# Optimization experiments

Measured on AMD Instinct MI355X. Metric: run time of the kernel, lower is better.

The kernel has to match this reference:

```python
import jax, jax.numpy as jnp
import numpy as np

K = 7            # kernel_size (odd)
R = K // 2       # neighborhood radius
NH = 16          # num_heads


def _starts(L):
    """NATTEN (dilation=1) window start and rpb start per query index."""
    i = jnp.arange(L)
    win = jnp.clip(i - R, 0, L - K)  # key-window start (window clamped inside image)
    pb = jnp.where(i < R, 2 * R - i, jnp.where(i + R >= L, L - 1 - i, R))
    return win, pb


def setup_inputs() -> dict:
    key = jax.random.key(0)
    ks = jax.random.split(key, 12)
    B, H, W, C = 2, 128, 128, 512
    std = 0.02
    return {
        "q": jax.random.normal(ks[0], (B, H, W, C), jnp.float32),
        "k": jax.random.normal(ks[1], (B, H, W, C), jnp.float32),
        "v": jax.random.normal(ks[2], (B, H, W, C), jnp.float32),
        "wq": jax.random.normal(ks[3], (C, C), jnp.float32) * std,
        "bq": jnp.zeros((C,), jnp.float32),
        "wk": jax.random.normal(ks[4], (C, C), jnp.float32) * std,
        "bk": jnp.zeros((C,), jnp.float32),
        "wv": jax.random.normal(ks[5], (C, C), jnp.float32) * std,
        "bv": jnp.zeros((C,), jnp.float32),
        "rpb": jax.random.normal(ks[6], (NH, 2 * K - 1, 2 * K - 1), jnp.float32) * std,
        "wo": jax.random.normal(ks[7], (C, C), jnp.float32) * std,
        "bo": jnp.zeros((C,), jnp.float32),
    }


def reference(q, k, v, wq, bq, wk, bk, wv, bv, rpb, wo, bo):
    B, H, W, C = q.shape
    hd = C // NH
    scale = hd ** -0.5

    def proj(x, w, b):
        y = x @ w.T + b  # torch nn.Linear
        return y.reshape(B, H, W, NH, hd).transpose(0, 3, 1, 2, 4)  # [B,nh,H,W,hd]

    qh = proj(q, wq, bq) * scale
    kh = proj(k, wk, bk)
    vh = proj(v, wv, bv)

    # H,W (128) >= window_size (7): torch padding branch is dead and omitted.
    sh, ph = _starts(H)
    sw, pw = _starts(W)

    # natten2dqkrpb: per-offset shifted-row/col gathers; never materialize
    # the dense [B,nh,H,W,k*k,hd] unfold.
    logits = []
    for a in range(K):
        kh_a = kh[:, :, sh + a]          # [B,nh,H,W,hd]
        rpb_a = rpb[:, ph + a]           # [nh,H,2K-1]
        for b in range(K):
            k_ab = kh_a[:, :, :, sw + b]             # [B,nh,H,W,hd]
            bias = rpb_a[:, :, pw + b]               # [nh,H,W]
            logits.append(jnp.einsum("bnhwd,bnhwd->bnhw", qh, k_ab) + bias[None])
    attn = jax.nn.softmax(jnp.stack(logits, axis=-1), axis=-1)  # [B,nh,H,W,K*K]

    # natten2dav
    x = jnp.zeros_like(qh)
    for a in range(K):
        vh_a = vh[:, :, sh + a]
        for b in range(K):
            v_ab = vh_a[:, :, :, sw + b]
            x = x + attn[..., a * K + b, None] * v_ab

    x = x.transpose(0, 2, 3, 1, 4).reshape(B, H, W, C)
    return x @ wo.T + bo
```

## Files before the change

kernel.cpp:

```cpp
#include <hip/hip_runtime.h>
#include <hip/hip_bf16.h>

typedef __attribute__((ext_vector_type(8))) _Float16       h8;
typedef __attribute__((ext_vector_type(2))) _Float16       h2;
typedef __attribute__((ext_vector_type(8))) unsigned short u16x8;
typedef __attribute__((ext_vector_type(4))) float          f4;
typedef __attribute__((ext_vector_type(4))) unsigned int   u32x4;
typedef __attribute__((ext_vector_type(2))) unsigned int   u32x2;

__device__ __forceinline__ h2 bch2(unsigned int w) { return __builtin_bit_cast(h2, w); }
__device__ __forceinline__ unsigned int pkrtz(float a, float b) {
    auto r = __builtin_amdgcn_cvt_pkrtz(a, b);
    return __builtin_bit_cast(unsigned int, r);
}
__device__ __forceinline__ void gload_lds16(const void* g, void* l) {
    __builtin_amdgcn_global_load_lds(
        (const __attribute__((address_space(1))) unsigned int*)g,
        (__attribute__((address_space(3))) unsigned int*)l, 16, 0, 0);
}

__global__ __launch_bounds__(256) void cvt_w4(const float* __restrict__ a,
                                              const float* __restrict__ b,
                                              const float* __restrict__ c,
                                              const float* __restrict__ d,
                                              unsigned short* __restrict__ o) {
    const int i   = (blockIdx.x * 256 + threadIdx.x) * 8;
    const int seg = i >> 18;
    const int off = i & 262143;
    const float* s = (seg == 0) ? a : (seg == 1) ? b : (seg == 2) ? c : d;
    f4 x0 = *(const f4*)(s + off);
    f4 x1 = *(const f4*)(s + off + 4);
    u32x4 t;
    t[0] = pkrtz(x0[0], x0[1]);
    t[1] = pkrtz(x0[2], x0[3]);
    t[2] = pkrtz(x1[0], x1[1]);
    t[3] = pkrtz(x1[2], x1[3]);
    *(u32x4*)(o + i) = t;
}

template <bool AF32, bool OF32>
__device__ __forceinline__ void gemm_body(const void* __restrict__ Ap,
                                          const unsigned short* __restrict__ Wb,
                                          const float* __restrict__ bias,
                                          void* __restrict__ Outp,
                                          float scale,
                                          unsigned char* lds) {
    constexpr int KD = 512, BK = 32, NT = KD / BK;
    constexpr int ASZ = AF32 ? 64 * BK * 4 : 64 * BK * 2;
    constexpr int WSZ = 512 * BK * 2;
    constexpr int STRIDE = ASZ + WSZ;

    const int tid  = threadIdx.x;
    const int lane = tid & 63;
    const int w    = tid >> 6;
    const size_t m0 = (size_t)blockIdx.x * 64;

    const float*          Af = (const float*)Ap;
    const unsigned short* Ab = (const unsigned short*)Ap;

    const int fr = lane & 15;
    const int j4 = lane >> 4;

    f4 acc[4][8];
#pragma unroll
    for (int i = 0; i < 4; ++i)
#pragma unroll
        for (int j = 0; j < 8; ++j) acc[i][j] = (f4)(0.0f);

    auto stage = [&](int t, int buf) {
        const int kt = t * BK;
        unsigned char* base = lds + buf * STRIDE;
        if constexpr (AF32) {
#pragma unroll
            for (int i = 0; i < 2; ++i) {
                const int f = i * 256 + tid;
                const int row = f >> 3, p = f & 7;
                const int s = p ^ (row & 7);
                gload_lds16(Af + (m0 + row) * KD + kt + s * 4, base + f * 16);
            }
        } else {
            const int f = tid;
            const int l = f ^ ((f >> 3) & 7);
            gload_lds16(Ab + (m0 + (l >> 2)) * KD + kt + (l & 3) * 8, base + f * 16);
        }
#pragma unroll
        for (int i = 0; i < 8; ++i) {
            const int f = i * 256 + tid;
            const int l = f ^ ((f >> 3) & 7);
            gload_lds16(Wb + (size_t)(l >> 2) * KD + kt + (l & 3) * 8,
                        base + ASZ + f * 16);
        }
    };

    stage(0, 0);
    stage(1, 1);

    for (int t = 0; t < NT; ++t) {
        const int buf = t & 1;
        unsigned char* base = lds + buf * STRIDE;
        if (t + 1 < NT) {
            if constexpr (AF32) asm volatile("s_waitcnt vmcnt(10)" ::: "memory");
            else                asm volatile("s_waitcnt vmcnt(9)"  ::: "memory");
        } else {
            asm volatile("s_waitcnt vmcnt(0)" ::: "memory");
        }
        __builtin_amdgcn_s_barrier();
        __builtin_amdgcn_sched_barrier(0);

        h8 af[4];
#pragma unroll
        for (int mi = 0; mi < 4; ++mi) {
            const int row = mi * 16 + fr;
            if constexpr (AF32) {
                const int r7 = row & 7;
                const int s0 = j4 * 2;
                f4 x0 = *(const f4*)(base + row * 128 + ((s0 ^ r7) << 4));
                f4 x1 = *(const f4*)(base + row * 128 + (((s0 + 1) ^ r7) << 4));
                u32x4 t4;
                t4[0] = pkrtz(x0[0], x0[1]);
                t4[1] = pkrtz(x0[2], x0[3]);
                t4[2] = pkrtz(x1[0], x1[1]);
                t4[3] = pkrtz(x1[2], x1[3]);
                af[mi] = __builtin_bit_cast(h8, t4);
            } else {
                const int L = (row << 2) | j4;
                const int P = L ^ ((L >> 3) & 7);
                af[mi] = *(const h8*)(base + (P << 4));
            }
        }
#pragma unroll
        for (int ni = 0; ni < 8; ++ni) {
            const int nrow = w * 128 + ni * 16 + fr;
            const int L = (nrow << 2) | j4;
            const int P = L ^ ((L >> 3) & 7);
            const h8 bf = *(const h8*)(base + ASZ + (P << 4));
#pragma unroll
            for (int mi = 0; mi < 4; ++mi)
                acc[mi][ni] = __builtin_amdgcn_mfma_f32_16x16x32_f16(
                    af[mi], bf, acc[mi][ni], 0, 0, 0);
        }

        __builtin_amdgcn_sched_barrier(0);
        __builtin_amdgcn_s_barrier();
        __builtin_amdgcn_sched_barrier(0);
        if (t + 2 < NT) stage(t + 2, buf);
    }

    const int rq = (lane >> 4) << 2;
#pragma unroll
    for (int ni = 0; ni < 8; ++ni) {
        const int   col = w * 128 + ni * 16 + fr;
        const float bv  = bias[col];
#pragma unroll
        for (int mi = 0; mi < 4; ++mi) {
            const size_t rbase = m0 + mi * 16 + rq;
#pragma unroll
            for (int r = 0; r < 4; ++r) {
                const float val = (acc[mi][ni][r] + bv) * scale;
                if constexpr (OF32) {
                    ((float*)Outp)[(rbase + r) * KD + col] = val;
                } else {
                    const _Float16 hv = (_Float16)val;
                    ((unsigned short*)Outp)[(rbase + r) * KD + col] =
                        __builtin_bit_cast(unsigned short, hv);
                }
            }
        }
    }
}

__global__ __launch_bounds__(256, 2) void gemm_proj3(const float* __restrict__ q,
                                                     const float* __restrict__ k,
                                                     const float* __restrict__ v,
                                                     const unsigned short* __restrict__ Wb,
                                                     const float* __restrict__ bq,
                                                     const float* __restrict__ bk,
                                                     const float* __restrict__ bv,
                                                     unsigned short* __restrict__ qh,
                                                     unsigned short* __restrict__ kh,
                                                     unsigned short* __restrict__ vh,
                                                     float scale) {
    extern __shared__ unsigned char lds[];
    const int by = blockIdx.y;
    const float*          A  = (by == 0) ? q  : (by == 1) ? k  : v;
    const float*          bi = (by == 0) ? bq : (by == 1) ? bk : bv;
    unsigned short*       O  = (by == 0) ? qh : (by == 1) ? kh : vh;
    gemm_body<true, false>(A, Wb + (size_t)by * 262144, bi, O,
                           (by == 0) ? scale : 1.0f, lds);
}

__global__ __launch_bounds__(256, 2) void gemm_outk(const unsigned short* __restrict__ Xb,
                                                    const unsigned short* __restrict__ Wb,
                                                    const float* __restrict__ bias,
                                                    float* __restrict__ Out) {
    extern __shared__ unsigned char lds[];
    gemm_body<false, true>(Xb, Wb, bias, Out, 1.0f, lds);
}

__global__ __launch_bounds__(256, 4) void natt(const unsigned short* __restrict__ qh,
                                               const unsigned short* __restrict__ kh,
                                               const unsigned short* __restrict__ vh,
                                               const float* __restrict__ rpb,
                                               unsigned short* __restrict__ xout) {
    constexpr int LDK = 40;
    __shared__ unsigned short KV[484][LDK];
    __shared__ float Rs[169];

    const int tid = threadIdx.x;
    const int h   = blockIdx.z & 15;
    const int b   = blockIdx.z >> 4;
    const int x0  = blockIdx.x * 16;
    const int y0  = blockIdx.y * 16;
    const int ux0 = min(max(x0 - 3, 0), 106);
    const int uy0 = min(max(y0 - 3, 0), 106);
    const int tx  = tid & 15;
    const int ty  = tid >> 4;
    const int x   = x0 + tx;
    const int y   = y0 + ty;

    if (tid < 169) Rs[tid] = rpb[h * 169 + tid];

    const long imgbase = (long)b * 128 * 128;

#pragma unroll 2
    for (int kk = tid; kk < 484; kk += 256) {
        const int ky = uy0 + kk / 22;
        const int kx = ux0 + kk % 22;
        const unsigned short* src = kh + (imgbase + ky * 128 + kx) * 512 + h * 32;
#pragma unroll
        for (int j = 0; j < 4; ++j)
            *(u16x8*)&KV[kk][j * 8] = *(const u16x8*)(src + j * 8);
    }

    const long pix = imgbase + y * 128 + x;
    const unsigned short* qp = qh + pix * 512 + h * 32;
    h2 qv[16];
    {
        const u32x4* q32 = (const u32x4*)qp;
#pragma unroll
        for (int j = 0; j < 4; ++j) {
            const u32x4 wv = q32[j];
#pragma unroll
            for (int e = 0; e < 4; ++e) qv[j * 4 + e] = bch2(wv[e]);
        }
    }

    const int myy = min(max(y - 3, 0), 121) - uy0;
    const int myx = min(max(x - 3, 0), 121) - ux0;
    const int pbY = (y < 3) ? (6 - y) : ((y >= 125) ? (127 - y) : 3);
    const int pbX = (x < 3) ? (6 - x) : ((x >= 125) ? (127 - x) : 3);

    __syncthreads();

    float logit[49];
#pragma unroll
    for (int a = 0; a < 7; ++a) {
        const int rowk = (myy + a) * 22 + myx;
#pragma unroll
        for (int c = 0; c < 7; ++c) {
            const u32x4* kp = (const u32x4*)&KV[rowk + c][0];
            float s0 = 0.f, s1 = 0.f;
#pragma unroll
            for (int j = 0; j < 4; ++j) {
                const u32x4 wv = kp[j];
                s0 = __builtin_amdgcn_fdot2(qv[4 * j + 0], bch2(wv[0]), s0, false);
                s1 = __builtin_amdgcn_fdot2(qv[4 * j + 1], bch2(wv[1]), s1, false);
                s0 = __builtin_amdgcn_fdot2(qv[4 * j + 2], bch2(wv[2]), s0, false);
                s1 = __builtin_amdgcn_fdot2(qv[4 * j + 3], bch2(wv[3]), s1, false);
            }
            logit[a * 7 + c] = s0 + s1 + Rs[(pbY + a) * 13 + pbX + c];
        }
    }

    float m = logit[0];
#pragma unroll
    for (int i = 1; i < 49; ++i) m = fmaxf(m, logit[i]);
    float sum = 0.f;
#pragma unroll
    for (int i = 0; i < 49; ++i) {
        float p = exp2f((logit[i] - m) * 1.4426950408889634f);
        logit[i] = p;
        sum += p;
    }
    const float rinv = 1.f / sum;
#pragma unroll
    for (int i = 0; i < 49; ++i) logit[i] *= rinv;

    __syncthreads();

#pragma unroll 2
    for (int kk = tid; kk < 484; kk += 256) {
        const int ky = uy0 + kk / 22;
        const int kx = ux0 + kk % 22;
        const unsigned short* src = vh + (imgbase + ky * 128 + kx) * 512 + h * 32;
#pragma unroll
        for (int j = 0; j < 4; ++j)
            *(u16x8*)&KV[kk][j * 8] = *(const u16x8*)(src + j * 8);
    }
    __syncthreads();

    float acc[32];
#pragma unroll
    for (int d = 0; d < 32; ++d) acc[d] = 0.f;
#pragma unroll
    for (int a = 0; a < 7; ++a) {
        const int rowk = (myy + a) * 22 + myx;
#pragma unroll
        for (int c = 0; c < 7; ++c) {
            const u32x4* vp = (const u32x4*)&KV[rowk + c][0];
            const float wgt = logit[a * 7 + c];
#pragma unroll
            for (int j = 0; j < 4; ++j) {
                const u32x4 wv = vp[j];
#pragma unroll
                for (int e = 0; e < 4; ++e) {
                    const h2 hv = bch2(wv[e]);
                    acc[8 * j + 2 * e]     = fmaf((float)hv[0], wgt, acc[8 * j + 2 * e]);
                    acc[8 * j + 2 * e + 1] = fmaf((float)hv[1], wgt, acc[8 * j + 2 * e + 1]);
                }
            }
        }
    }

    unsigned short* op = xout + pix * 512 + h * 32;
#pragma unroll
    for (int j = 0; j < 4; ++j) {
        u32x2 p;
        p[0] = pkrtz(acc[8 * j + 0], acc[8 * j + 1]);
        p[1] = pkrtz(acc[8 * j + 2], acc[8 * j + 3]);
        u32x2 p2;
        p2[0] = pkrtz(acc[8 * j + 4], acc[8 * j + 5]);
        p2[1] = pkrtz(acc[8 * j + 6], acc[8 * j + 7]);
        *(u32x2*)(op + j * 8)     = p;
        *(u32x2*)(op + j * 8 + 4) = p2;
    }
}

extern "C" void kernel_launch(void* const* d_in, const int* in_sizes, int n_in,
                              void* d_out, int out_size, void* d_ws, size_t ws_size,
                              hipStream_t stream) {
    const float* q   = (const float*)d_in[0];
    const float* k   = (const float*)d_in[1];
    const float* v   = (const float*)d_in[2];
    const float* wq  = (const float*)d_in[3];
    const float* bq  = (const float*)d_in[4];
    const float* wk  = (const float*)d_in[5];
    const float* bk  = (const float*)d_in[6];
    const float* wv  = (const float*)d_in[7];
    const float* bv  = (const float*)d_in[8];
    const float* rpb = (const float*)d_in[9];
    const float* wo  = (const float*)d_in[10];
    const float* bo  = (const float*)d_in[11];

    const long P = 2l * 128 * 128;
    unsigned short* qh = (unsigned short*)d_ws;
    unsigned short* kh = qh + P * 512;
    unsigned short* vh = kh + P * 512;
    unsigned short* xb = vh + P * 512;
    unsigned short* Wb = xb + P * 512;

    const float scale = 0.17677669529663687f;
    const size_t smemF = 2 * (64 * 32 * 4 + 512 * 32 * 2);
    const size_t smemB = 2 * (64 * 32 * 2 + 512 * 32 * 2);

    cvt_w4<<<512, 256, 0, stream>>>(wq, wk, wv, wo, Wb);

    gemm_proj3<<<dim3(512, 3, 1), 256, smemF, stream>>>(
        q, k, v, Wb, bq, bk, bv, qh, kh, vh, scale);

    natt<<<dim3(8, 8, 32), 256, 0, stream>>>(qh, kh, vh, rpb, xb);

    gemm_outk<<<512, 256, smemB, stream>>>(xb, Wb + 786432, bo, (float*)d_out);
}
```

Measured before the change: 222.1 us.

## Split GEMM N dimension into 256-wide tiles and launch projections separately

The projection and output GEMMs now tile 64x256 instead of 64x512, adding a grid dimension over N so each block holds half the weight tile and half the accumulators. This lowers LDS and register use per block, allowing three blocks per CU, and doubles the number of blocks. The fused three-way projection kernel is split into three separate launches. In exchange, each A tile (fp32 activations) is loaded and converted twice, and there are extra kernel launches.

Measured after the change: 239.7 us. 1.08x slower.

```diff
diff --git a/kernel.cpp b/kernel.cpp
--- a/kernel.cpp
+++ b/kernel.cpp
@@ -39,21 +39,23 @@
 }
 
 template <bool AF32, bool OF32>
-__device__ __forceinline__ void gemm_body(const void* __restrict__ Ap,
-                                          const unsigned short* __restrict__ Wb,
-                                          const float* __restrict__ bias,
-                                          void* __restrict__ Outp,
-                                          float scale,
-                                          unsigned char* lds) {
+__global__ __launch_bounds__(256, 3) void gemm_ns(const void* __restrict__ Ap,
+                                                  const unsigned short* __restrict__ Wb,
+                                                  const float* __restrict__ bias,
+                                                  void* __restrict__ Outp,
+                                                  float scale) {
     constexpr int KD = 512, BK = 32, NT = KD / BK;
     constexpr int ASZ = AF32 ? 64 * BK * 4 : 64 * BK * 2;
-    constexpr int WSZ = 512 * BK * 2;
+    constexpr int WSZ = 256 * BK * 2;
     constexpr int STRIDE = ASZ + WSZ;
+    constexpr int NSTG = AF32 ? 6 : 5;
+    extern __shared__ unsigned char lds[];
 
     const int tid  = threadIdx.x;
     const int lane = tid & 63;
     const int w    = tid >> 6;
-    const size_t m0 = (size_t)blockIdx.x * 64;
+    const int n0   = blockIdx.x * 256;
+    const size_t m0 = (size_t)blockIdx.y * 64;
 
     const float*          Af = (const float*)Ap;
     const unsigned short* Ab = (const unsigned short*)Ap;
@@ -61,11 +63,11 @@
     const int fr = lane & 15;
     const int j4 = lane >> 4;
 
-    f4 acc[4][8];
+    f4 acc[4][4];
 #pragma unroll
     for (int i = 0; i < 4; ++i)
 #pragma unroll
-        for (int j = 0; j < 8; ++j) acc[i][j] = (f4)(0.0f);
+        for (int j = 0; j < 4; ++j) acc[i][j] = (f4)(0.0f);
 
     auto stage = [&](int t, int buf) {
         const int kt = t * BK;
@@ -84,10 +86,10 @@
             gload_lds16(Ab + (m0 + (l >> 2)) * KD + kt + (l & 3) * 8, base + f * 16);
         }
 #pragma unroll
-        for (int i = 0; i < 8; ++i) {
+        for (int i = 0; i < 4; ++i) {
             const int f = i * 256 + tid;
             const int l = f ^ ((f >> 3) & 7);
-            gload_lds16(Wb + (size_t)(l >> 2) * KD + kt + (l & 3) * 8,
+            gload_lds16(Wb + (size_t)(n0 + (l >> 2)) * KD + kt + (l & 3) * 8,
                         base + ASZ + f * 16);
         }
     };
@@ -99,8 +101,7 @@
         const int buf = t & 1;
         unsigned char* base = lds + buf * STRIDE;
         if (t + 1 < NT) {
-            if constexpr (AF32) asm volatile("s_waitcnt vmcnt(10)" ::: "memory");
-            else                asm volatile("s_waitcnt vmcnt(9)"  ::: "memory");
+            asm volatile("s_waitcnt vmcnt(%0)" :: "i"(NSTG) : "memory");
         } else {
             asm volatile("s_waitcnt vmcnt(0)" ::: "memory");
         }
@@ -129,8 +130,8 @@
             }
         }
 #pragma unroll
-        for (int ni = 0; ni < 8; ++ni) {
-            const int nrow = w * 128 + ni * 16 + fr;
+        for (int ni = 0; ni < 4; ++ni) {
+            const int nrow = w * 64 + ni * 16 + fr;
             const int L = (nrow << 2) | j4;
             const int P = L ^ ((L >> 3) & 7);
             const h8 bf = *(const h8*)(base + ASZ + (P << 4));
@@ -148,8 +149,8 @@
 
     const int rq = (lane >> 4) << 2;
 #pragma unroll
-    for (int ni = 0; ni < 8; ++ni) {
-        const int   col = w * 128 + ni * 16 + fr;
+    for (int ni = 0; ni < 4; ++ni) {
+        const int   col = n0 + w * 64 + ni * 16 + fr;
         const float bv  = bias[col];
 #pragma unroll
         for (int mi = 0; mi < 4; ++mi) {
@@ -167,34 +168,6 @@
             }
         }
     }
-}
-
-__global__ __launch_bounds__(256, 2) void gemm_proj3(const float* __restrict__ q,
-                                                     const float* __restrict__ k,
-                                                     const float* __restrict__ v,
-                                                     const unsigned short* __restrict__ Wb,
-                                                     const float* __restrict__ bq,
-                                                     const float* __restrict__ bk,
-                                                     const float* __restrict__ bv,
-                                                     unsigned short* __restrict__ qh,
-                                                     unsigned short* __restrict__ kh,
-                                                     unsigned short* __restrict__ vh,
-                                                     float scale) {
-    extern __shared__ unsigned char lds[];
-    const int by = blockIdx.y;
-    const float*          A  = (by == 0) ? q  : (by == 1) ? k  : v;
-    const float*          bi = (by == 0) ? bq : (by == 1) ? bk : bv;
-    unsigned short*       O  = (by == 0) ? qh : (by == 1) ? kh : vh;
-    gemm_body<true, false>(A, Wb + (size_t)by * 262144, bi, O,
-                           (by == 0) ? scale : 1.0f, lds);
-}
-
-__global__ __launch_bounds__(256, 2) void gemm_outk(const unsigned short* __restrict__ Xb,
-                                                    const unsigned short* __restrict__ Wb,
-                                                    const float* __restrict__ bias,
-                                                    float* __restrict__ Out) {
-    extern __shared__ unsigned char lds[];
-    gemm_body<false, true>(Xb, Wb, bias, Out, 1.0f, lds);
 }
 
 __global__ __launch_bounds__(256, 4) void natt(const unsigned short* __restrict__ qh,
@@ -360,15 +333,17 @@
     unsigned short* Wb = xb + P * 512;
 
     const float scale = 0.17677669529663687f;
-    const size_t smemF = 2 * (64 * 32 * 4 + 512 * 32 * 2);
-    const size_t smemB = 2 * (64 * 32 * 2 + 512 * 32 * 2);
+    const size_t smemF = 2 * (64 * 32 * 4 + 256 * 32 * 2);
+    const size_t smemB = 2 * (64 * 32 * 2 + 256 * 32 * 2);
+    const dim3 gg(2, 512, 1);
 
     cvt_w4<<<512, 256, 0, stream>>>(wq, wk, wv, wo, Wb);
 
-    gemm_proj3<<<dim3(512, 3, 1), 256, smemF, stream>>>(
-        q, k, v, Wb, bq, bk, bv, qh, kh, vh, scale);
+    gemm_ns<true, false><<<gg, 256, smemF, stream>>>(q, Wb,          bq, qh, scale);
+    gemm_ns<true, false><<<gg, 256, smemF, stream>>>(k, Wb + 262144, bk, kh, 1.0f);
+    gemm_ns<true, false><<<gg, 256, smemF, stream>>>(v, Wb + 524288, bv, vh, 1.0f);
 
     natt<<<dim3(8, 8, 32), 256, 0, stream>>>(qh, kh, vh, rpb, xb);
 
-    gemm_outk<<<512, 256, smemB, stream>>>(xb, Wb + 786432, bo, (float*)d_out);
-}
+    gemm_ns<false, true><<<gg, 256, smemB, stream>>>(xb, Wb + 786432, bo, (float*)d_out, 1.0f);
+}
```

## Pre-convert q/k/v to fp16 and run separate fp16 projection GEMMs

Applied to the files above, without the earlier changes.

Adds a standalone kernel that converts the fp32 q, k and v activations to fp16 into scratch buffers, reusing the xb workspace and the output buffer. The fused three-way fp32-input projection GEMM becomes three launches of a single fp16-input GEMM template. The aim is to take the fp32 staging and in-loop packing out of the GEMM main loop and shrink its LDS footprint. In exchange it adds a full extra read and write pass over the activations and splits one large launch into three smaller ones.

Result: slower. 260.7 us (+17.4%).

```diff
diff --git a/kernel.cpp b/kernel.cpp
--- a/kernel.cpp
+++ b/kernel.cpp
@@ -38,26 +38,44 @@
     *(u32x4*)(o + i) = t;
 }
 
-template <bool AF32, bool OF32>
-__device__ __forceinline__ void gemm_body(const void* __restrict__ Ap,
-                                          const unsigned short* __restrict__ Wb,
-                                          const float* __restrict__ bias,
-                                          void* __restrict__ Outp,
-                                          float scale,
-                                          unsigned char* lds) {
+__global__ __launch_bounds__(256) void cvt_x3(const float* __restrict__ q,
+                                              const float* __restrict__ k,
+                                              const float* __restrict__ v,
+                                              unsigned short* __restrict__ o0,
+                                              unsigned short* __restrict__ o1,
+                                              unsigned short* __restrict__ o2) {
+    const long i  = ((long)blockIdx.x * 256 + threadIdx.x) * 8;
+    const int seg = (int)(i >> 24);
+    const long off = i & 0xFFFFFFl;
+    const float* s       = (seg == 0) ? q  : (seg == 1) ? k  : v;
+    unsigned short* dst  = (seg == 0) ? o0 : (seg == 1) ? o1 : o2;
+    f4 x0 = *(const f4*)(s + off);
+    f4 x1 = *(const f4*)(s + off + 4);
+    u32x4 t;
+    t[0] = pkrtz(x0[0], x0[1]);
+    t[1] = pkrtz(x0[2], x0[3]);
+    t[2] = pkrtz(x1[0], x1[1]);
+    t[3] = pkrtz(x1[2], x1[3]);
+    *(u32x4*)(dst + off) = t;
+}
+
+template <bool OF32>
+__global__ __launch_bounds__(256, 2) void gemm16(const unsigned short* __restrict__ Ab,
+                                                 const unsigned short* __restrict__ Wb,
+                                                 const float* __restrict__ bias,
+                                                 void* __restrict__ Outp,
+                                                 float scale) {
     constexpr int KD = 512, BK = 32, NT = KD / BK;
-    constexpr int ASZ = AF32 ? 64 * BK * 4 : 64 * BK * 2;
+    constexpr int ASZ = 64 * BK * 2;
     constexpr int WSZ = 512 * BK * 2;
     constexpr int STRIDE = ASZ + WSZ;
+    extern __shared__ unsigned char lds[];
 
     const int tid  = threadIdx.x;
     const int lane = tid & 63;
     const int w    = tid >> 6;
     const size_t m0 = (size_t)blockIdx.x * 64;
 
-    const float*          Af = (const float*)Ap;
-    const unsigned short* Ab = (const unsigned short*)Ap;
-
     const int fr = lane & 15;
     const int j4 = lane >> 4;
 
@@ -70,15 +88,7 @@
     auto stage = [&](int t, int buf) {
         const int kt = t * BK;
         unsigned char* base = lds + buf * STRIDE;
-        if constexpr (AF32) {
-#pragma unroll
-            for (int i = 0; i < 2; ++i) {
-                const int f = i * 256 + tid;
-                const int row = f >> 3, p = f & 7;
-                const int s = p ^ (row & 7);
-                gload_lds16(Af + (m0 + row) * KD + kt + s * 4, base + f * 16);
-            }
-        } else {
+        {
             const int f = tid;
             const int l = f ^ ((f >> 3) & 7);
             gload_lds16(Ab + (m0 + (l >> 2)) * KD + kt + (l & 3) * 8, base + f * 16);
@@ -99,8 +109,7 @@
         const int buf = t & 1;
         unsigned char* base = lds + buf * STRIDE;
         if (t + 1 < NT) {
-            if constexpr (AF32) asm volatile("s_waitcnt vmcnt(10)" ::: "memory");
-            else                asm volatile("s_waitcnt vmcnt(9)"  ::: "memory");
+            asm volatile("s_waitcnt vmcnt(9)" ::: "memory");
         } else {
             asm volatile("s_waitcnt vmcnt(0)" ::: "memory");
         }
@@ -111,22 +120,9 @@
 #pragma unroll
         for (int mi = 0; mi < 4; ++mi) {
             const int row = mi * 16 + fr;
-            if constexpr (AF32) {
-                const int r7 = row & 7;
-                const int s0 = j4 * 2;
-                f4 x0 = *(const f4*)(base + row * 128 + ((s0 ^ r7) << 4));
-                f4 x1 = *(const f4*)(base + row * 128 + (((s0 + 1) ^ r7) << 4));
-                u32x4 t4;
-                t4[0] = pkrtz(x0[0], x0[1]);
-                t4[1] = pkrtz(x0[2], x0[3]);
-                t4[2] = pkrtz(x1[0], x1[1]);
-                t4[3] = pkrtz(x1[2], x1[3]);
-                af[mi] = __builtin_bit_cast(h8, t4);
-            } else {
-                const int L = (row << 2) | j4;
-                const int P = L ^ ((L >> 3) & 7);
-                af[mi] = *(const h8*)(base + (P << 4));
-            }
+            const int L = (row << 2) | j4;
+            const int P = L ^ ((L >> 3) & 7);
+            af[mi] = *(const h8*)(base + (P << 4));
         }
 #pragma unroll
         for (int ni = 0; ni < 8; ++ni) {
@@ -167,34 +163,6 @@
             }
         }
     }
-}
-
-__global__ __launch_bounds__(256, 2) void gemm_proj3(const float* __restrict__ q,
-                                                     const float* __restrict__ k,
-                                                     const float* __restrict__ v,
-                                                     const unsigned short* __restrict__ Wb,
-                                                     const float* __restrict__ bq,
-                                                     const float* __restrict__ bk,
-                                                     const float* __restrict__ bv,
-                                                     unsigned short* __restrict__ qh,
-                                                     unsigned short* __restrict__ kh,
-                                                     unsigned short* __restrict__ vh,
-                                                     float scale) {
-    extern __shared__ unsigned char lds[];
-    const int by = blockIdx.y;
-    const float*          A  = (by == 0) ? q  : (by == 1) ? k  : v;
-    const float*          bi = (by == 0) ? bq : (by == 1) ? bk : bv;
-    unsigned short*       O  = (by == 0) ? qh : (by == 1) ? kh : vh;
-    gemm_body<true, false>(A, Wb + (size_t)by * 262144, bi, O,
-                           (by == 0) ? scale : 1.0f, lds);
-}
-
-__global__ __launch_bounds__(256, 2) void gemm_outk(const unsigned short* __restrict__ Xb,
-                                                    const unsigned short* __restrict__ Wb,
-                                                    const float* __restrict__ bias,
-                                                    float* __restrict__ Out) {
-    extern __shared__ unsigned char lds[];
-    gemm_body<false, true>(Xb, Wb, bias, Out, 1.0f, lds);
 }
 
 __global__ __launch_bounds__(256, 4) void natt(const unsigned short* __restrict__ qh,
@@ -359,16 +327,21 @@
     unsigned short* xb = vh + P * 512;
     unsigned short* Wb = xb + P * 512;
 
+    unsigned short* q16 = xb;
+    unsigned short* k16 = (unsigned short*)d_out;
+    unsigned short* v16 = k16 + 16777216;
+
     const float scale = 0.17677669529663687f;
-    const size_t smemF = 2 * (64 * 32 * 4 + 512 * 32 * 2);
-    const size_t smemB = 2 * (64 * 32 * 2 + 512 * 32 * 2);
+    const size_t smem = 2 * (64 * 32 * 2 + 512 * 32 * 2);
 
     cvt_w4<<<512, 256, 0, stream>>>(wq, wk, wv, wo, Wb);
-
-    gemm_proj3<<<dim3(512, 3, 1), 256, smemF, stream>>>(
-        q, k, v, Wb, bq, bk, bv, qh, kh, vh, scale);
+    cvt_x3<<<24576, 256, 0, stream>>>(q, k, v, q16, k16, v16);
+
+    gemm16<false><<<512, 256, smem, stream>>>(q16, Wb,          bq, qh, scale);
+    gemm16<false><<<512, 256, smem, stream>>>(k16, Wb + 262144, bk, kh, 1.0f);
+    gemm16<false><<<512, 256, smem, stream>>>(v16, Wb + 524288, bv, vh, 1.0f);
 
     natt<<<dim3(8, 8, 32), 256, 0, stream>>>(qh, kh, vh, rpb, xb);
 
-    gemm_outk<<<512, 256, smemB, stream>>>(xb, Wb + 786432, bo, (float*)d_out);
-}
+    gemm16<true><<<512, 256, smem, stream>>>(xb, Wb + 786432, bo, (float*)d_out, 1.0f);
+}
```

## Replace QKV projection GEMM with 128x256-tile kernel converting A to fp16 in LDS

Applied to the files above, without the earlier changes.

Replaces the QKV projection kernel (64-row tiles spanning all 512 output columns, fp32 A staged in LDS) with a new 512-thread kernel using 128x256 tiles. The fp32 activations are loaded into registers, packed to fp16 and written to a padded LDS buffer. Weights go through swizzled direct global-to-LDS loads with double buffering and explicit waitcnt/barrier scheduling. This halves A-tile LDS footprint and changes the work split (2 N-tiles per M-block, so A is read twice from global) in exchange for better wave count and LDS reuse.

New measurement: 224.1 us. About the same (+0.9%).

```diff
diff --git a/kernel.cpp b/kernel.cpp
--- a/kernel.cpp
+++ b/kernel.cpp
@@ -38,6 +38,139 @@
     *(u32x4*)(o + i) = t;
 }
 
+__global__ __launch_bounds__(512, 4) void gemm_p2(const float* __restrict__ q,
+                                                  const float* __restrict__ k,
+                                                  const float* __restrict__ v,
+                                                  const unsigned short* __restrict__ Wb,
+                                                  const float* __restrict__ bq,
+                                                  const float* __restrict__ bk,
+                                                  const float* __restrict__ bv,
+                                                  unsigned short* __restrict__ qh,
+                                                  unsigned short* __restrict__ kh,
+                                                  unsigned short* __restrict__ vh,
+                                                  float scale) {
+    constexpr int KD = 512, BK = 32, NT = KD / BK;
+    constexpr int APAD = 40;
+    constexpr int ASZ  = 128 * APAD * 2;
+    constexpr int WSZ  = 256 * BK * 2;
+    constexpr int STRIDE = ASZ + WSZ;
+    __shared__ unsigned char lds[2 * STRIDE];
+
+    const int z = blockIdx.z;
+    const float* Af           = (z == 0) ? q  : (z == 1) ? k  : v;
+    const float* bias         = (z == 0) ? bq : (z == 1) ? bk : bv;
+    unsigned short* Out       = (z == 0) ? qh : (z == 1) ? kh : vh;
+    const unsigned short* W   = Wb + (size_t)z * 262144;
+    const float fscale        = (z == 0) ? scale : 1.0f;
+
+    const int tid  = threadIdx.x;
+    const int lane = tid & 63;
+    const int w    = tid >> 6;
+    const int wm   = w >> 2;
+    const int wn   = w & 3;
+    const int n0   = blockIdx.x * 256;
+    const size_t m0 = (size_t)blockIdx.y * 128;
+
+    const int fr = lane & 15;
+    const int j4 = lane >> 4;
+    const int arow = tid >> 2;
+    const int acol = (tid & 3) * 8;
+
+    f4 acc[4][4];
+#pragma unroll
+    for (int i = 0; i < 4; ++i)
+#pragma unroll
+        for (int j = 0; j < 4; ++j) acc[i][j] = (f4)(0.0f);
+
+    auto wissue = [&](int t) {
+        unsigned char* base = lds + (t & 1) * STRIDE + ASZ;
+        const int kt = t * BK;
+#pragma unroll
+        for (int i = 0; i < 2; ++i) {
+            const int f = i * 512 + tid;
+            const int l = f ^ ((f >> 3) & 7);
+            gload_lds16(W + (size_t)(n0 + (l >> 2)) * KD + kt + (l & 3) * 8,
+                        base + f * 16);
+        }
+    };
+    auto aload = [&](int t, f4& r0, f4& r1) {
+        const float* p = Af + (m0 + arow) * KD + t * BK + acol;
+        r0 = *(const f4*)p;
+        r1 = *(const f4*)(p + 4);
+    };
+    auto awrite = [&](int t, const f4& r0, const f4& r1) {
+        u32x4 t4;
+        t4[0] = pkrtz(r0[0], r0[1]);
+        t4[1] = pkrtz(r0[2], r0[3]);
+        t4[2] = pkrtz(r1[0], r1[1]);
+        t4[3] = pkrtz(r1[2], r1[3]);
+        *(u32x4*)(lds + (t & 1) * STRIDE + arow * (APAD * 2) + acol * 2) = t4;
+    };
+
+    {
+        f4 a0, a1;
+        aload(0, a0, a1); awrite(0, a0, a1);
+        aload(1, a0, a1); awrite(1, a0, a1);
+    }
+    wissue(0);
+    wissue(1);
+    asm volatile("s_waitcnt vmcnt(2)" ::: "memory");
+    asm volatile("s_waitcnt lgkmcnt(0)" ::: "memory");
+
+    for (int t = 0; t < NT; ++t) {
+        unsigned char* base = lds + (t & 1) * STRIDE;
+        f4 r0, r1;
+        if (t + 2 < NT) aload(t + 2, r0, r1);
+        __builtin_amdgcn_s_barrier();
+        __builtin_amdgcn_sched_barrier(0);
+
+        h8 af[4];
+#pragma unroll
+        for (int mi = 0; mi < 4; ++mi)
+            af[mi] = *(const h8*)(base + (wm * 64 + mi * 16 + fr) * (APAD * 2)
+                                  + j4 * 16);
+#pragma unroll
+        for (int ni = 0; ni < 4; ++ni) {
+            const int row = wn * 64 + ni * 16 + fr;
+            const int L = (row << 2) | j4;
+            const int P = L ^ ((L >> 3) & 7);
+            const h8 wf = *(const h8*)(base + ASZ + (P << 4));
+#pragma unroll
+            for (int mi = 0; mi < 4; ++mi)
+                acc[mi][ni] = __builtin_amdgcn_mfma_f32_16x16x32_f16(
+                    af[mi], wf, acc[mi][ni], 0, 0, 0);
+        }
+
+        __builtin_amdgcn_sched_barrier(0);
+        __builtin_amdgcn_s_barrier();
+        __builtin_amdgcn_sched_barrier(0);
+        asm volatile("s_waitcnt vmcnt(0)" ::: "memory");
+        if (t + 2 < NT) {
+            awrite(t + 2, r0, r1);
+            wissue(t + 2);
+        }
+        asm volatile("s_waitcnt lgkmcnt(0)" ::: "memory");
+        __builtin_amdgcn_sched_barrier(0);
+    }
+
+    const int rq = (lane >> 4) << 2;
+#pragma unroll
+    for (int ni = 0; ni < 4; ++ni) {
+        const int   col = n0 + wn * 64 + ni * 16 + fr;
+        const float bv  = bias[col];
+#pragma unroll
+        for (int mi = 0; mi < 4; ++mi) {
+            const size_t rbase = m0 + wm * 64 + mi * 16 + rq;
+#pragma unroll
+            for (int r = 0; r < 4; ++r) {
+                const float val = (acc[mi][ni][r] + bv) * fscale;
+                const _Float16 hv = (_Float16)val;
+                Out[(rbase + r) * KD + col] = __builtin_bit_cast(unsigned short, hv);
+            }
+        }
+    }
+}
+
 template <bool AF32, bool OF32>
 __device__ __forceinline__ void gemm_body(const void* __restrict__ Ap,
                                           const unsigned short* __restrict__ Wb,
@@ -169,26 +302,6 @@
     }
 }
 
-__global__ __launch_bounds__(256, 2) void gemm_proj3(const float* __restrict__ q,
-                                                     const float* __restrict__ k,
-                                                     const float* __restrict__ v,
-                                                     const unsigned short* __restrict__ Wb,
-                                                     const float* __restrict__ bq,
-                                                     const float* __restrict__ bk,
-                                                     const float* __restrict__ bv,
-                                                     unsigned short* __restrict__ qh,
-                                                     unsigned short* __restrict__ kh,
-                                                     unsigned short* __restrict__ vh,
-                                                     float scale) {
-    extern __shared__ unsigned char lds[];
-    const int by = blockIdx.y;
-    const float*          A  = (by == 0) ? q  : (by == 1) ? k  : v;
-    const float*          bi = (by == 0) ? bq : (by == 1) ? bk : bv;
-    unsigned short*       O  = (by == 0) ? qh : (by == 1) ? kh : vh;
-    gemm_body<true, false>(A, Wb + (size_t)by * 262144, bi, O,
-                           (by == 0) ? scale : 1.0f, lds);
-}
-
 __global__ __launch_bounds__(256, 2) void gemm_outk(const unsigned short* __restrict__ Xb,
                                                     const unsigned short* __restrict__ Wb,
                                                     const float* __restrict__ bias,
@@ -360,12 +473,11 @@
     unsigned short* Wb = xb + P * 512;
 
     const float scale = 0.17677669529663687f;
-    const size_t smemF = 2 * (64 * 32 * 4 + 512 * 32 * 2);
     const size_t smemB = 2 * (64 * 32 * 2 + 512 * 32 * 2);
 
     cvt_w4<<<512, 256, 0, stream>>>(wq, wk, wv, wo, Wb);
 
-    gemm_proj3<<<dim3(512, 3, 1), 256, smemF, stream>>>(
+    gemm_p2<<<dim3(2, 256, 3), 512, 0, stream>>>(
         q, k, v, Wb, bq, bk, bv, qh, kh, vh, scale);
 
     natt<<<dim3(8, 8, 32), 256, 0, stream>>>(qh, kh, vh, rpb, xb);
```
